# Optimization experiments

Hardware: AMD Instinct MI355X
Metric: run time of the kernel (lower is better)

## Reference

```python
import jax, jax.numpy as jnp
import numpy as np

VOCAB = 128
N_LAYERS = 4
HEAD_DIM = 128
N_HEADS = 16
PAD = 127
HIDDEN = N_HEADS * HEAD_DIM
B, S = 1, 2048
SCALE = 1.0 / float(np.sqrt(HEAD_DIM))


def _intervals(boundary):
    # torch: interval = cumsum(boundary)+1; shifted = roll(1); shifted[:,0]=interval[:,0]
    idx = jnp.cumsum(boundary.astype(jnp.int32), axis=-1) + 1
    sh = jnp.roll(idx, 1, axis=-1)
    return sh.at[:, 0].set(idx[:, 0])


def _build_mask(tokens, segment_mask, specials_mask):
    # Combined causal & padding & word & segment mask, cache_size=0, distances=0.
    word_int = _intervals(specials_mask)            # [B,S]
    seg_bound = ~segment_mask                       # [B,S]
    seg_int = _intervals(seg_bound)                 # [B,S]
    q = jnp.arange(S)[:, None]
    kv = jnp.arange(S)[None, :]
    causal = q >= kv                                # [S,S]
    dist_neg = (q - kv) < 0                         # mask_*_distance = 0 term
    nonpad = tokens != PAD                          # [B,S]
    padm = nonpad[:, :, None] & nonpad[:, None, :]  # [B,S,S]
    wordm = specials_mask[:, None, :] | dist_neg[None] | (word_int[:, :, None] == word_int[:, None, :])
    segm = seg_bound[:, None, :] | dist_neg[None] | (seg_int[:, :, None] == seg_int[:, None, :])
    return causal[None] & padm & wordm & segm       # [B,S,S]


def _attention(h, mask):
    # q=k=v=h (no projections in DummyModel); flex_attention default scale 1/sqrt(D)
    x = h.reshape(B, S, N_HEADS, HEAD_DIM)
    scores = jnp.einsum('bqhd,bkhd->bhqk', x, x) * SCALE
    neg = jnp.finfo(scores.dtype).min
    scores = jnp.where(mask[:, None], scores, neg)
    probs = jax.nn.softmax(scores, axis=-1)
    # fully-masked rows (e.g. padding queries) -> zero output, matching flex_attention
    row_valid = jnp.any(mask, axis=-1)              # [B,S]
    probs = jnp.where(row_valid[:, None, :, None], probs, 0.0)
    out = jnp.einsum('bhqk,bkhd->bqhd', probs, x)
    return out.reshape(B, S, HIDDEN)


def setup_inputs() -> dict:
    key = jax.random.key(0)
    k1, k2, k3, k4, k5, k6 = jax.random.split(key, 6)
    tokens = jax.random.randint(k1, (B, S), 0, PAD)          # 0..126, no pad tokens
    segment_mask = jax.random.bernoulli(k2, 0.98, (B, S))
    specials_mask = jax.random.bernoulli(k3, 0.2, (B, S))    # True = word boundary/special
    emb_w = jax.random.normal(k4, (VOCAB, HIDDEN), jnp.float32) * 0.02
    lm_w = jax.random.normal(k5, (VOCAB, HIDDEN), jnp.float32) * 0.02
    lm_b = jnp.zeros((VOCAB,), jnp.float32)
    seg_w = jax.random.normal(k6, (2, HIDDEN), jnp.float32) * 0.02
    seg_b = jnp.zeros((2,), jnp.float32)
    return {"tokens": tokens, "segment_mask": segment_mask, "specials_mask": specials_mask,
            "emb_w": emb_w, "lm_w": lm_w, "lm_b": lm_b, "seg_w": seg_w, "seg_b": seg_b}


def reference(tokens, segment_mask, specials_mask, emb_w, lm_w, lm_b, seg_w, seg_b):
    mask = _build_mask(tokens, segment_mask, specials_mask)
    hidden = emb_w[tokens]                                   # [B,S,HIDDEN]
    for _ in range(N_LAYERS):
        hidden = _attention(hidden, mask)
    logits = hidden @ lm_w.T + lm_b                          # [B,S,VOCAB]
    logits_segment = hidden @ seg_w.T + seg_b                # [B,S,2]
    return logits, logits_segment
```

## Files before the change

kernel.cpp:

```cpp
#include <hip/hip_runtime.h>

#define S 2048
#define HID 2048
#define NH 16
#define DH 128
#define VOC 128
#define LCAP 128
#define K2EXP 0.12752551286084112f
#define RTHR 62.0f
#define NEGS -3.0e38f

typedef __bf16 bf16_t;
typedef __attribute__((ext_vector_type(8))) __bf16 bf16x8;
typedef __attribute__((ext_vector_type(4))) __bf16 bf16x4;
typedef __attribute__((ext_vector_type(4))) float f32x4;
typedef __attribute__((ext_vector_type(16))) float f32x16;

typedef __attribute__((address_space(1))) unsigned int guint;
typedef __attribute__((address_space(3))) unsigned int luint;

#define MFMA16 __builtin_amdgcn_mfma_f32_16x16x32_bf16
#define MFMA32 __builtin_amdgcn_mfma_f32_32x32x16_bf16

__device__ __forceinline__ void gl_lds16(const void* g, void* l) {
  __builtin_amdgcn_global_load_lds((guint*)(unsigned long long)g,
                                   (luint*)(unsigned)(unsigned long long)l,
                                   16, 0, 0);
}

__device__ __forceinline__ unsigned cvtpk(float lo, float hi) {
  unsigned r;
  asm("v_cvt_pk_bf16_f32 %0, %1, %2" : "=v"(r) : "v"(lo), "v"(hi));
  return r;
}
__device__ __forceinline__ void plswap(unsigned& a, unsigned& b) {
  asm volatile("v_permlane32_swap_b32 %0, %1" : "+v"(a), "+v"(b));
}
__device__ __forceinline__ bf16x8 mk8(unsigned d0, unsigned d1, unsigned d2, unsigned d3) {
  union { unsigned u[4]; bf16x8 v; } x;
  x.u[0] = d0; x.u[1] = d1; x.u[2] = d2; x.u[3] = d3;
  return x.v;
}

__global__ __launch_bounds__(256) void maskprep2(const int* __restrict__ tokens,
                                                 const unsigned char* __restrict__ seg,
                                                 const unsigned char* __restrict__ spc,
                                                 int4* __restrict__ mi,
                                                 int* __restrict__ lq,
                                                 unsigned long long* __restrict__ lmask,
                                                 int2* __restrict__ smeta) {
  __shared__ int ssp[257], ssg[257], smw[257], sms[257], sfl[257];
  __shared__ int fpre[2048];
  __shared__ int ns64[64];
  __shared__ unsigned long long lmk[32];
  __shared__ int cdet[2];
  int t = threadIdx.x;
  if (t < 2) cdet[t] = 0;
  if (t < 32) lmk[t] = 0ull;
  __syncthreads();
  {
    int nz = ((t & 3) != 0 && seg[t]) ? 1 : 0;
    int fc = ((t & 3) == 3 && seg[t] == 0x3f) ? 1 : 0;
    if (nz) atomicAdd(&cdet[0], 1);
    if (fc) atomicAdd(&cdet[1], 1);
  }
  __syncthreads();
  int lay = (cdet[1] > 8) ? 2 : ((cdet[0] > 4) ? 1 : 0);
  auto getb = [&](const unsigned char* p, int i) -> int {
    if (lay == 1) return p[i] != 0;
    if (lay == 2) return ((const float*)p)[i] != 0.f;
    return ((const int*)p)[i] != 0;
  };
  int base = t * 8;
  int spv[8], sgv[8], npv[8], fv[8];
  int a = 0, b = 0, mw = 0, ms = 0, fs = 0;
  for (int j = 0; j < 8; j++) {
    int i = base + j;
    spv[j] = getb(spc, i);
    sgv[j] = 1 - getb(seg, i);
    npv[j] = (tokens[i] != 127) ? 1 : 0;
    fv[j] = spv[j] & sgv[j] & npv[j];
    a += spv[j]; b += sgv[j]; fs += fv[j];
    if (i >= 1 && spv[j]) mw = (i + 1 > mw) ? i + 1 : mw;
    if (i >= 1 && sgv[j]) ms = (i + 1 > ms) ? i + 1 : ms;
  }
  ssp[t + 1] = a; ssg[t + 1] = b; smw[t + 1] = mw; sms[t + 1] = ms; sfl[t + 1] = fs;
  if (t == 0) { ssp[0] = 0; ssg[0] = 0; smw[0] = 0; sms[0] = 0; sfl[0] = 0; }
  __syncthreads();
  for (int off = 1; off < 256; off <<= 1) {
    int v0 = 0, v1 = 0, v2 = 0, v3 = 0, v4 = 0;
    if (t + 1 > off) { v0 = ssp[t+1-off]; v1 = ssg[t+1-off]; v2 = smw[t+1-off]; v3 = sms[t+1-off]; v4 = sfl[t+1-off]; }
    __syncthreads();
    ssp[t + 1] += v0; ssg[t + 1] += v1;
    if (v2 > smw[t + 1]) smw[t + 1] = v2;
    if (v3 > sms[t + 1]) sms[t + 1] = v3;
    sfl[t + 1] += v4;
    __syncthreads();
  }
  if ((t & 3) == 0) {
    int ws = smw[t], ss = sms[t];
    ns64[t >> 2] = ws < ss ? ws : ss;
  }
  int esp = ssp[t], esg = ssg[t], ef = sfl[t];
  for (int j = 0; j < 8; j++) {
    int i = base + j;
    int wint = (i == 0) ? (1 + spv[j]) : (1 + esp);
    int sint = (i == 0) ? (1 + sgv[j]) : (1 + esg);
    mi[i] = make_int4(npv[j] | (spv[j] << 1) | (sgv[j] << 2), wint, sint, 0);
    fpre[i] = ef;
    int lqv = (fv[j] && ef < LCAP) ? ef : -1;
    lq[i] = lqv;
    if (lqv >= 0) atomicOr(&lmk[i >> 6], 1ull << (i & 63));
    esp += spv[j]; esg += sgv[j]; ef += fv[j];
  }
  __syncthreads();
  if (t < 32) lmask[t] = lmk[t];
  if (t < 64) {
    int nsTile = ns64[t] >> 5;
    int lc = fpre[nsTile * 32];
    if (lc > LCAP) lc = LCAP;
    smeta[t] = make_int2(nsTile, lc);
  }
}

__global__ __launch_bounds__(256) void bitgen(const int4* __restrict__ mi,
                                              unsigned* __restrict__ cmask) {
  __shared__ int4 km[32];
  int w = blockIdx.x;
  int t = threadIdx.x;
  int q = blockIdx.y * 256 + t;
  if (t < 32) km[t] = mi[w * 32 + t];
  __syncthreads();
  int4 mq = mi[q];
  unsigned word = 0;
  #pragma unroll
  for (int j = 0; j < 32; j++) {
    int kv = w * 32 + j;
    int4 mk = km[j];
    bool v = ((mq.x & mk.x) & 1) &&
             ((mk.x & 2) || (mq.y == mk.y)) &&
             ((mk.x & 4) || (mq.z == mk.z)) &&
             (kv <= q);
    word |= (v ? 1u : 0u) << j;
  }
  cmask[(size_t)w * S + q] = word;
}

__device__ __forceinline__ void store_h_hT(bf16x8 ob[4], bf16_t* tile, int q0, int h,
                                           int ql, int d0, int tid,
                                           bf16_t* __restrict__ hb, bf16_t* __restrict__ hbT) {
  #pragma unroll
  for (int i = 0; i < 4; i++)
    *(bf16x8*)(hb + (size_t)(q0 + ql) * HID + h * DH + d0 + i * 8) = ob[i];
  #pragma unroll
  for (int i = 0; i < 4; i++)
    #pragma unroll
    for (int j = 0; j < 8; j++) tile[ql * 136 + d0 + i * 8 + j] = ob[i][j];
  __syncthreads();
  int dT = tid >> 1, qh = (tid & 1) * 32;
  bf16x8 tb[4];
  #pragma unroll
  for (int i = 0; i < 4; i++)
    #pragma unroll
    for (int j = 0; j < 8; j++) tb[i][j] = tile[(qh + i * 8 + j) * 136 + dT];
  #pragma unroll
  for (int i = 0; i < 4; i++)
    *(bf16x8*)(hbT + (size_t)(h * DH + dT) * S + q0 + qh + i * 8) = tb[i];
}

__global__ __launch_bounds__(256) void embedT(const int* __restrict__ tokens,
                                              const float* __restrict__ emb,
                                              const int* __restrict__ lq,
                                              const unsigned long long* __restrict__ lmask,
                                              bf16_t* __restrict__ hb, bf16_t* __restrict__ hbT,
                                              bf16_t* __restrict__ hbL, bf16_t* __restrict__ hbLT) {
  __shared__ bf16_t tile[64 * 136];
  int tid = threadIdx.x;
  int q0 = blockIdx.x * 64, h = blockIdx.y;
  int ql = tid >> 2, d0 = (tid & 3) * 32;
  int tok = tokens[q0 + ql];
  const float4* src = (const float4*)(emb + (size_t)tok * HID + h * DH + d0);
  bf16x8 ob[4];
  #pragma unroll
  for (int i = 0; i < 8; i++) {
    float4 f = src[i];
    ob[i >> 1][(i & 1) * 4 + 0] = (bf16_t)f.x;
    ob[i >> 1][(i & 1) * 4 + 1] = (bf16_t)f.y;
    ob[i >> 1][(i & 1) * 4 + 2] = (bf16_t)f.z;
    ob[i >> 1][(i & 1) * 4 + 3] = (bf16_t)f.w;
  }
  store_h_hT(ob, tile, q0, h, ql, d0, tid, hb, hbT);
  unsigned long long lm = lmask[q0 >> 6];
  while (lm) {
    int r = __builtin_ctzll(lm);
    lm &= lm - 1;
    int li = lq[q0 + r];
    if (li >= 0 && tid < 128) {
      bf16_t vv = tile[r * 136 + tid];
      hbL[(size_t)li * HID + h * DH + tid] = vv;
      hbLT[((size_t)(h * DH + tid)) * LCAP + li] = vv;
    }
  }
}

__global__ __launch_bounds__(64, 2) void attn7(const bf16_t* __restrict__ hb,
                                               const bf16_t* __restrict__ hbT,
                                               const bf16_t* __restrict__ hbL,
                                               const bf16_t* __restrict__ hbLT,
                                               const unsigned* __restrict__ cmask,
                                               const int4* __restrict__ mi,
                                               const int2* __restrict__ smeta,
                                               const int* __restrict__ lq,
                                               const unsigned long long* __restrict__ lmask,
                                               bf16_t* __restrict__ ob,
                                               bf16_t* __restrict__ obT,
                                               bf16_t* __restrict__ obL,
                                               bf16_t* __restrict__ obLT,
                                               int writeT) {
  __shared__ __align__(16) char lds_raw[32768];

  int h = blockIdx.x, st = blockIdx.y;
  int2 sm = smeta[st];
  int nsT = sm.x, lcount = sm.y;
  int nNear = st + 1 - nsT;
  int nLT = (lcount + 31) >> 5;
  int nIter = nNear + nLT;

  int l = threadIdx.x, l31 = l & 31, hi = l >> 5;
  int q0 = 32 * st, q = q0 + l31;
  int npq = mi[q].x & 1;

  bf16x8 qf[8];
  {
    const bf16_t* hq = hb + (size_t)q * HID + h * DH;
    #pragma unroll
    for (int ks = 0; ks < 8; ks++) qf[ks] = *(const bf16x8*)(hq + ks * 16 + hi * 8);
  }

  f32x16 acc[4];
  #pragma unroll
  for (int i = 0; i < 4; i++)
    #pragma unroll
    for (int r = 0; r < 16; r++) acc[i][r] = 0.f;
  float m = -1e30f, lsum = 0.f;
  int swz = l31 & 7;

  auto STAGE = [&](int i, int b) {
    const bf16_t* Kbase; const bf16_t* Vbase; size_t Vstr;
    if (i < nNear) {
      int kv0 = (nsT + i) * 32;
      Kbase = hb + (size_t)kv0 * HID + h * DH;
      Vbase = hbT + (size_t)(h * DH) * S + kv0; Vstr = S;
    } else {
      int j0 = (i - nNear) * 32;
      Kbase = hbL + (size_t)j0 * HID + h * DH;
      Vbase = hbLT + (size_t)(h * DH) * LCAP + j0; Vstr = LCAP;
    }
    bf16_t* Kb = (bf16_t*)(lds_raw + b * 16384);
    bf16_t* Vb = (bf16_t*)(lds_raw + b * 16384 + 8192);
    #pragma unroll
    for (int i2 = 0; i2 < 8; i2++) {
      int rowK = i2 * 4 + (l >> 4); int chK = (l & 15) ^ (rowK & 7);
      gl_lds16(Kbase + (size_t)rowK * HID + chK * 8, Kb + i2 * 512);
    }
    #pragma unroll
    for (int i2 = 0; i2 < 8; i2++) {
      int rowV = i2 * 16 + (l >> 2); int chV = (l & 3) ^ (rowV & 3);
      gl_lds16(Vbase + (size_t)rowV * Vstr + chV * 8, Vb + i2 * 512);
    }
  };

  auto getmask = [&](int i) -> unsigned {
    if (i < nNear) return cmask[(size_t)(nsT + i) * S + q];
    int rem = lcount - (i - nNear) * 32;
    unsigned w0 = (rem >= 32) ? 0xffffffffu : ((rem <= 0) ? 0u : ((1u << rem) - 1u));
    return npq ? w0 : 0u;
  };

  STAGE(0, 0);
  for (int i = 0; i < nIter; i++) {
    int b = i & 1;
    if (i + 1 < nIter) {
      STAGE(i + 1, b ^ 1);
      asm volatile("s_waitcnt vmcnt(16)" ::: "memory");
    } else {
      asm volatile("s_waitcnt vmcnt(0)" ::: "memory");
    }
    unsigned w0 = getmask(i);

    if (__any(w0 != 0u)) {
      const bf16_t* Kb = (const bf16_t*)(lds_raw + b * 16384);
      const bf16_t* Vb = (const bf16_t*)(lds_raw + b * 16384 + 8192);
      f32x16 s;
      #pragma unroll
      for (int r = 0; r < 16; r++) s[r] = 0.f;
      const bf16_t* kp = Kb + l31 * 128;
      #pragma unroll
      for (int ks = 0; ks < 8; ks++) {
        bf16x8 kf = *(const bf16x8*)(kp + (((2 * ks + hi) ^ swz) * 8));
        s = MFMA32(kf, qf[ks], s, 0, 0, 0);
      }

      float sv[16];
      float mx = NEGS;
      #pragma unroll
      for (int r = 0; r < 16; r++) {
        int bit = (r & 3) + 8 * (r >> 2) + 4 * hi;
        sv[r] = ((w0 >> bit) & 1u) ? s[r] : NEGS;
        mx = fmaxf(mx, sv[r]);
      }
      mx = fmaxf(mx, __shfl_xor(mx, 32, 64));
      if (__any(mx > m + RTHR)) {
        float mn = fmaxf(m, mx);
        float al = exp2f((m - mn) * K2EXP);
        m = mn; lsum *= al;
        #pragma unroll
        for (int r = 0; r < 16; r++) {
          float alr = __shfl(al, (r & 3) + 8 * (r >> 2) + 4 * hi, 64);
          #pragma unroll
          for (int d = 0; d < 4; d++) acc[d][r] *= alr;
        }
      }
      float mk = m * K2EXP;
      float p[16], ps = 0.f;
      #pragma unroll
      for (int r = 0; r < 16; r++) {
        p[r] = exp2f(__builtin_fmaf(sv[r], K2EXP, -mk));
        ps += p[r];
      }
      ps += __shfl_xor(ps, 32, 64);
      lsum += ps;

      bf16x8 pa[2];
      {
        unsigned a0 = cvtpk(p[0], p[1]),   a1 = cvtpk(p[2], p[3]);
        unsigned b0 = cvtpk(p[4], p[5]),   b1 = cvtpk(p[6], p[7]);
        unsigned a2 = cvtpk(p[8], p[9]),   a3 = cvtpk(p[10], p[11]);
        unsigned b2 = cvtpk(p[12], p[13]), b3 = cvtpk(p[14], p[15]);
        plswap(a0, b0); plswap(a1, b1); plswap(a2, b2); plswap(a3, b3);
        pa[0] = mk8(a0, a1, b0, b1);
        pa[1] = mk8(a2, a3, b2, b3);
      }

      #pragma unroll
      for (int db = 0; db < 4; db++) {
        const bf16_t* vr = Vb + (32 * db + l31) * 32;
        #pragma unroll
        for (int ks = 0; ks < 2; ks++) {
          bf16x8 vf = *(const bf16x8*)(vr + (((2 * ks + hi) ^ (l31 & 3)) * 8));
          acc[db] = MFMA32(pa[ks], vf, acc[db], 0, 0, 0);
        }
      }
    }
  }

  bf16_t* tl = (bf16_t*)lds_raw;
  float inv = (lsum > 0.f) ? 1.f / lsum : 0.f;
  #pragma unroll
  for (int r = 0; r < 16; r++) {
    int qr = (r & 3) + 8 * (r >> 2) + 4 * hi;
    float ivr = __shfl(inv, qr, 64);
    #pragma unroll
    for (int db = 0; db < 4; db++)
      tl[qr * 132 + db * 32 + l31] = (bf16_t)(acc[db][r] * ivr);
  }
  {
    int row = l >> 1, hf = l & 1;
    #pragma unroll
    for (int k = 0; k < 8; k++) {
      bf16x8 v = *(const bf16x8*)(tl + row * 132 + hf * 64 + k * 8);
      *(bf16x8*)(ob + (size_t)(q0 + row) * HID + h * DH + hf * 64 + k * 8) = v;
    }
  }
  if (writeT) {
    #pragma unroll
    for (int half = 0; half < 2; half++) {
      int dd = l + 64 * half;
      #pragma unroll
      for (int c = 0; c < 4; c++) {
        bf16x8 v;
        #pragma unroll
        for (int e = 0; e < 8; e++) v[e] = tl[(c * 8 + e) * 132 + dd];
        *(bf16x8*)(obT + (size_t)(h * DH + dd) * S + q0 + c * 8) = v;
      }
    }
    unsigned lm32 = (unsigned)(lmask[st >> 1] >> ((st & 1) * 32));
    while (lm32) {
      int r = __builtin_ctz(lm32);
      lm32 &= lm32 - 1;
      int li = lq[q0 + r];
      if (li >= 0) {
        #pragma unroll
        for (int half = 0; half < 2; half++) {
          int dd = l + 64 * half;
          bf16_t vv = tl[r * 132 + dd];
          obL[(size_t)li * HID + h * DH + dd] = vv;
          obLT[((size_t)(h * DH + dd)) * LCAP + li] = vv;
        }
      }
    }
  }
}

__global__ __launch_bounds__(256) void wcvt(const float* __restrict__ w, bf16_t* __restrict__ wb) {
  int i = blockIdx.x * 256 + threadIdx.x;
  float4 f = ((const float4*)w)[i];
  bf16x4 v;
  v[0] = (bf16_t)f.x; v[1] = (bf16_t)f.y; v[2] = (bf16_t)f.z; v[3] = (bf16_t)f.w;
  *(bf16x4*)(wb + (size_t)i * 4) = v;
}

__global__ __launch_bounds__(256) void lmseg_head(const bf16_t* __restrict__ hb,
                                                  const bf16_t* __restrict__ wbf,
                                                  const float* __restrict__ bias,
                                                  const float* __restrict__ sw,
                                                  const float* __restrict__ sb,
                                                  float* __restrict__ out,
                                                  float* __restrict__ outseg) {
  __shared__ float red[4][16][130];
  int tid = threadIdx.x;
  int w = tid >> 6, l = tid & 63, l16 = l & 15, g = l >> 4;
  int t0 = blockIdx.x * 16;
  f32x4 acc[8];
  #pragma unroll
  for (int i = 0; i < 8; i++) acc[i] = (f32x4){0.f, 0.f, 0.f, 0.f};
  const bf16_t* arow = hb + (size_t)(t0 + l16) * HID + w * 512;
  for (int k0 = 0; k0 < 512; k0 += 32) {
    bf16x8 af = *(const bf16x8*)(arow + k0 + g * 8);
    #pragma unroll
    for (int vt = 0; vt < 8; vt++) {
      bf16x8 bf_ = *(const bf16x8*)(wbf + (size_t)(vt * 16 + l16) * HID + w * 512 + k0 + g * 8);
      acc[vt] = MFMA16(af, bf_, acc[vt], 0, 0, 0);
    }
  }
  #pragma unroll
  for (int vt = 0; vt < 8; vt++)
    #pragma unroll
    for (int r = 0; r < 4; r++)
      red[w][4 * g + r][vt * 16 + l16] = acc[vt][r];
  __syncthreads();
  int q = tid >> 4, vc = (tid & 15) * 8;
  #pragma unroll
  for (int j = 0; j < 8; j++) {
    float s = red[0][q][vc + j] + red[1][q][vc + j] + red[2][q][vc + j] + red[3][q][vc + j];
    out[(size_t)(t0 + q) * VOC + vc + j] = s + bias[vc + j];
  }
  {
    int c = tid & 15;
    const bf16_t* hrow = hb + (size_t)(t0 + q) * HID + c * 128;
    float s0 = 0.f, s1 = 0.f;
    #pragma unroll
    for (int i = 0; i < 16; i++) {
      bf16x8 v = *(const bf16x8*)(hrow + i * 8);
      const float4* w0p = (const float4*)(sw + c * 128 + i * 8);
      const float4* w1p = (const float4*)(sw + HID + c * 128 + i * 8);
      float4 x0 = w0p[0], x1 = w0p[1], y0 = w1p[0], y1 = w1p[1];
      s0 += (float)v[0]*x0.x + (float)v[1]*x0.y + (float)v[2]*x0.z + (float)v[3]*x0.w
          + (float)v[4]*x1.x + (float)v[5]*x1.y + (float)v[6]*x1.z + (float)v[7]*x1.w;
      s1 += (float)v[0]*y0.x + (float)v[1]*y0.y + (float)v[2]*y0.z + (float)v[3]*y0.w
          + (float)v[4]*y1.x + (float)v[5]*y1.y + (float)v[6]*y1.z + (float)v[7]*y1.w;
    }
    #pragma unroll
    for (int off = 1; off < 16; off <<= 1) {
      s0 += __shfl_xor(s0, off, 64);
      s1 += __shfl_xor(s1, off, 64);
    }
    if (c == 0) {
      outseg[(size_t)(t0 + q) * 2] = s0 + sb[0];
      outseg[(size_t)(t0 + q) * 2 + 1] = s1 + sb[1];
    }
  }
}

extern "C" void kernel_launch(void* const* d_in, const int* in_sizes, int n_in,
                              void* d_out, int out_size, void* d_ws, size_t ws_size,
                              hipStream_t stream) {
  const int* tokens = (const int*)d_in[0];
  const unsigned char* seg = (const unsigned char*)d_in[1];
  const unsigned char* spc = (const unsigned char*)d_in[2];
  const float* emb_w = (const float*)d_in[3];
  const float* lm_w = (const float*)d_in[4];
  const float* lm_b = (const float*)d_in[5];
  const float* seg_w = (const float*)d_in[6];
  const float* seg_b = (const float*)d_in[7];

  char* ws = (char*)d_ws;
  int4* mi = (int4*)ws;
  unsigned* cmask = (unsigned*)(ws + (1u << 20));
  int* lq = (int*)(ws + (1u << 20) + (512u << 10));
  unsigned long long* lmask = (unsigned long long*)(ws + (1u << 20) + (520u << 10));
  int2* smeta = (int2*)(ws + (1u << 20) + (524u << 10));
  bf16_t* wbf = (bf16_t*)(ws + (2u << 20));
  bf16_t* hbLA  = (bf16_t*)(ws + (3u << 20));
  bf16_t* hbLTA = (bf16_t*)(ws + (3u << 20) + (512u << 10));
  bf16_t* hbLB  = (bf16_t*)(ws + (4u << 20));
  bf16_t* hbLTB = (bf16_t*)(ws + (4u << 20) + (512u << 10));
  bf16_t* hbA  = (bf16_t*)(ws + (8u << 20));
  bf16_t* hbTA = (bf16_t*)(ws + (16u << 20));
  bf16_t* hbB  = (bf16_t*)(ws + (24u << 20));
  bf16_t* hbTB = (bf16_t*)(ws + (32u << 20));
  float* out = (float*)d_out;

  maskprep2<<<1, 256, 0, stream>>>(tokens, seg, spc, mi, lq, lmask, smeta);
  bitgen<<<dim3(64, 8), 256, 0, stream>>>(mi, cmask);
  embedT<<<dim3(S / 64, NH), 256, 0, stream>>>(tokens, emb_w, lq, lmask, hbA, hbTA, hbLA, hbLTA);

  bf16_t* cur = hbA;   bf16_t* curT = hbTA;
  bf16_t* nxt = hbB;   bf16_t* nxtT = hbTB;
  bf16_t* curL = hbLA; bf16_t* curLT = hbLTA;
  bf16_t* nxtL = hbLB; bf16_t* nxtLT = hbLTB;
  for (int L = 0; L < 4; L++) {
    attn7<<<dim3(NH, 64), 64, 0, stream>>>(cur, curT, curL, curLT, cmask, mi, smeta, lq, lmask,
                                           nxt, nxtT, nxtL, nxtLT, (L < 3) ? 1 : 0);
    bf16_t* t1 = cur; cur = nxt; nxt = t1;
    bf16_t* t2 = curT; curT = nxtT; nxtT = t2;
    bf16_t* t3 = curL; curL = nxtL; nxtL = t3;
    bf16_t* t4 = curLT; curLT = nxtLT; nxtLT = t4;
  }

  wcvt<<<(VOC * HID / 4) / 256, 256, 0, stream>>>(lm_w, wbf);
  lmseg_head<<<S / 16, 256, 0, stream>>>(cur, wbf, lm_b, seg_w, seg_b, out, out + (size_t)S * VOC);
}
```

Measured before the change: 147.6 us.

## Store V as pre-swizzled contiguous 32x128 tiles per head

Replaces the globally transposed hidden-state copy (hbT, stride S) with a tiled layout in which each head's 32-token V tile is stored contiguously, already in the XOR-swizzled LDS order. Attention staging then does linear 16-byte global-to-LDS loads instead of strided row gathers, and the producer kernels (embed and the attention epilogue) write tiles in that layout. The aim is better coalescing and fewer memory transactions for V loads. The cost is a more complex transpose-and-swizzle in the writers and a changed output store pattern.

```diff
diff --git a/kernel.cpp b/kernel.cpp
--- a/kernel.cpp
+++ b/kernel.cpp
@@ -41,6 +41,7 @@
   x.u[0] = d0; x.u[1] = d1; x.u[2] = d2; x.u[3] = d3;
   return x.v;
 }
+
 
 __global__ __launch_bounds__(256) void maskprep2(const int* __restrict__ tokens,
                                                  const unsigned char* __restrict__ seg,
@@ -146,34 +147,12 @@
   cmask[(size_t)w * S + q] = word;
 }
 
-__device__ __forceinline__ void store_h_hT(bf16x8 ob[4], bf16_t* tile, int q0, int h,
-                                           int ql, int d0, int tid,
-                                           bf16_t* __restrict__ hb, bf16_t* __restrict__ hbT) {
-  #pragma unroll
-  for (int i = 0; i < 4; i++)
-    *(bf16x8*)(hb + (size_t)(q0 + ql) * HID + h * DH + d0 + i * 8) = ob[i];
-  #pragma unroll
-  for (int i = 0; i < 4; i++)
-    #pragma unroll
-    for (int j = 0; j < 8; j++) tile[ql * 136 + d0 + i * 8 + j] = ob[i][j];
-  __syncthreads();
-  int dT = tid >> 1, qh = (tid & 1) * 32;
-  bf16x8 tb[4];
-  #pragma unroll
-  for (int i = 0; i < 4; i++)
-    #pragma unroll
-    for (int j = 0; j < 8; j++) tb[i][j] = tile[(qh + i * 8 + j) * 136 + dT];
-  #pragma unroll
-  for (int i = 0; i < 4; i++)
-    *(bf16x8*)(hbT + (size_t)(h * DH + dT) * S + q0 + qh + i * 8) = tb[i];
-}
-
-__global__ __launch_bounds__(256) void embedT(const int* __restrict__ tokens,
-                                              const float* __restrict__ emb,
-                                              const int* __restrict__ lq,
-                                              const unsigned long long* __restrict__ lmask,
-                                              bf16_t* __restrict__ hb, bf16_t* __restrict__ hbT,
-                                              bf16_t* __restrict__ hbL, bf16_t* __restrict__ hbLT) {
+__global__ __launch_bounds__(256) void embedT2(const int* __restrict__ tokens,
+                                               const float* __restrict__ emb,
+                                               const int* __restrict__ lq,
+                                               const unsigned long long* __restrict__ lmask,
+                                               bf16_t* __restrict__ hb, bf16_t* __restrict__ vtb,
+                                               bf16_t* __restrict__ hbL, bf16_t* __restrict__ vtbL) {
   __shared__ bf16_t tile[64 * 136];
   int tid = threadIdx.x;
   int q0 = blockIdx.x * 64, h = blockIdx.y;
@@ -189,7 +168,26 @@
     ob[i >> 1][(i & 1) * 4 + 2] = (bf16_t)f.z;
     ob[i >> 1][(i & 1) * 4 + 3] = (bf16_t)f.w;
   }
-  store_h_hT(ob, tile, q0, h, ql, d0, tid, hb, hbT);
+  #pragma unroll
+  for (int i = 0; i < 4; i++)
+    *(bf16x8*)(hb + (size_t)(q0 + ql) * HID + h * DH + d0 + i * 8) = ob[i];
+  #pragma unroll
+  for (int i = 0; i < 4; i++)
+    #pragma unroll
+    for (int j = 0; j < 8; j++) tile[ql * 136 + d0 + i * 8 + j] = ob[i][j];
+  __syncthreads();
+  {
+    int tl = tid >> 7, d = tid & 127;
+    bf16_t* vt = vtb + ((size_t)(h * 64) + 2 * blockIdx.x + tl) * 4096;
+    #pragma unroll
+    for (int c = 0; c < 4; c++) {
+      bf16x8 v;
+      #pragma unroll
+      for (int e = 0; e < 8; e++)
+        v[e] = tile[(32 * tl + 8 * (c ^ (d & 3)) + e) * 136 + d];
+      *(bf16x8*)(vt + d * 32 + c * 8) = v;
+    }
+  }
   unsigned long long lm = lmask[q0 >> 6];
   while (lm) {
     int r = __builtin_ctzll(lm);
@@ -198,24 +196,24 @@
     if (li >= 0 && tid < 128) {
       bf16_t vv = tile[r * 136 + tid];
       hbL[(size_t)li * HID + h * DH + tid] = vv;
-      hbLT[((size_t)(h * DH + tid)) * LCAP + li] = vv;
-    }
-  }
-}
-
-__global__ __launch_bounds__(64, 2) void attn7(const bf16_t* __restrict__ hb,
-                                               const bf16_t* __restrict__ hbT,
+      vtbL[((size_t)(h * 4) + (li >> 5)) * 4096 + tid * 32 + (((li & 31) >> 3) ^ (tid & 3)) * 8 + (li & 7)] = vv;
+    }
+  }
+}
+
+__global__ __launch_bounds__(64, 2) void attn8(const bf16_t* __restrict__ hb,
+                                               const bf16_t* __restrict__ vtb,
                                                const bf16_t* __restrict__ hbL,
-                                               const bf16_t* __restrict__ hbLT,
+                                               const bf16_t* __restrict__ vtbL,
                                                const unsigned* __restrict__ cmask,
                                                const int4* __restrict__ mi,
                                                const int2* __restrict__ smeta,
                                                const int* __restrict__ lq,
                                                const unsigned long long* __restrict__ lmask,
                                                bf16_t* __restrict__ ob,
-                                               bf16_t* __restrict__ obT,
+                                               bf16_t* __restrict__ ovtb,
                                                bf16_t* __restrict__ obL,
-                                               bf16_t* __restrict__ obLT,
+                                               bf16_t* __restrict__ ovtbL,
                                                int writeT) {
   __shared__ __align__(16) char lds_raw[32768];
 
@@ -246,15 +244,15 @@
   int swz = l31 & 7;
 
   auto STAGE = [&](int i, int b) {
-    const bf16_t* Kbase; const bf16_t* Vbase; size_t Vstr;
+    const bf16_t* Kbase; const bf16_t* Vtile;
     if (i < nNear) {
-      int kv0 = (nsT + i) * 32;
-      Kbase = hb + (size_t)kv0 * HID + h * DH;
-      Vbase = hbT + (size_t)(h * DH) * S + kv0; Vstr = S;
+      int t = nsT + i;
+      Kbase = hb + (size_t)(t * 32) * HID + h * DH;
+      Vtile = vtb + ((size_t)(h * 64) + t) * 4096;
     } else {
-      int j0 = (i - nNear) * 32;
-      Kbase = hbL + (size_t)j0 * HID + h * DH;
-      Vbase = hbLT + (size_t)(h * DH) * LCAP + j0; Vstr = LCAP;
+      int j = i - nNear;
+      Kbase = hbL + (size_t)(j * 32) * HID + h * DH;
+      Vtile = vtbL + ((size_t)(h * 4) + j) * 4096;
     }
     bf16_t* Kb = (bf16_t*)(lds_raw + b * 16384);
     bf16_t* Vb = (bf16_t*)(lds_raw + b * 16384 + 8192);
@@ -264,10 +262,8 @@
       gl_lds16(Kbase + (size_t)rowK * HID + chK * 8, Kb + i2 * 512);
     }
     #pragma unroll
-    for (int i2 = 0; i2 < 8; i2++) {
-      int rowV = i2 * 16 + (l >> 2); int chV = (l & 3) ^ (rowV & 3);
-      gl_lds16(Vbase + (size_t)rowV * Vstr + chV * 8, Vb + i2 * 512);
-    }
+    for (int i2 = 0; i2 < 8; i2++)
+      gl_lds16(Vtile + i2 * 512 + l * 8, Vb + i2 * 512);
   };
 
   auto getmask = [&](int i) -> unsigned {
@@ -365,24 +361,27 @@
       tl[qr * 132 + db * 32 + l31] = (bf16_t)(acc[db][r] * ivr);
   }
   {
-    int row = l >> 1, hf = l & 1;
-    #pragma unroll
-    for (int k = 0; k < 8; k++) {
-      bf16x8 v = *(const bf16x8*)(tl + row * 132 + hf * 64 + k * 8);
-      *(bf16x8*)(ob + (size_t)(q0 + row) * HID + h * DH + hf * 64 + k * 8) = v;
+    int c4 = l & 3;
+    #pragma unroll
+    for (int g = 0; g < 2; g++) {
+      int row = g * 16 + (l >> 2);
+      #pragma unroll
+      for (int k = 0; k < 4; k++) {
+        bf16x8 v = *(const bf16x8*)(tl + row * 132 + c4 * 32 + k * 8);
+        *(bf16x8*)(ob + (size_t)(q0 + row) * HID + h * DH + c4 * 32 + k * 8) = v;
+      }
     }
   }
   if (writeT) {
-    #pragma unroll
-    for (int half = 0; half < 2; half++) {
-      int dd = l + 64 * half;
-      #pragma unroll
-      for (int c = 0; c < 4; c++) {
-        bf16x8 v;
-        #pragma unroll
-        for (int e = 0; e < 8; e++) v[e] = tl[(c * 8 + e) * 132 + dd];
-        *(bf16x8*)(obT + (size_t)(h * DH + dd) * S + q0 + c * 8) = v;
-      }
+    bf16_t* vt = ovtb + ((size_t)(h * 64) + st) * 4096;
+    #pragma unroll
+    for (int s = 0; s < 8; s++) {
+      int d = s * 16 + (l >> 2);
+      bf16x8 v;
+      #pragma unroll
+      for (int e = 0; e < 8; e++)
+        v[e] = tl[(8 * ((l & 3) ^ (d & 3)) + e) * 132 + d];
+      *(bf16x8*)(vt + s * 512 + l * 8) = v;
     }
     unsigned lm32 = (unsigned)(lmask[st >> 1] >> ((st & 1) * 32));
     while (lm32) {
@@ -395,7 +394,7 @@
           int dd = l + 64 * half;
           bf16_t vv = tl[r * 132 + dd];
           obL[(size_t)li * HID + h * DH + dd] = vv;
-          obLT[((size_t)(h * DH + dd)) * LCAP + li] = vv;
+          ovtbL[((size_t)(h * 4) + (li >> 5)) * 4096 + dd * 32 + (((li & 31) >> 3) ^ (dd & 3)) * 8 + (li & 7)] = vv;
         }
       }
     }
@@ -492,30 +491,30 @@
   int2* smeta = (int2*)(ws + (1u << 20) + (524u << 10));
   bf16_t* wbf = (bf16_t*)(ws + (2u << 20));
   bf16_t* hbLA  = (bf16_t*)(ws + (3u << 20));
-  bf16_t* hbLTA = (bf16_t*)(ws + (3u << 20) + (512u << 10));
-  bf16_t* hbLB  = (bf16_t*)(ws + (4u << 20));
-  bf16_t* hbLTB = (bf16_t*)(ws + (4u << 20) + (512u << 10));
+  bf16_t* hbLB  = (bf16_t*)(ws + (3u << 20) + (512u << 10));
+  bf16_t* vtbLA = (bf16_t*)(ws + (4u << 20));
+  bf16_t* vtbLB = (bf16_t*)(ws + (4u << 20) + (512u << 10));
   bf16_t* hbA  = (bf16_t*)(ws + (8u << 20));
-  bf16_t* hbTA = (bf16_t*)(ws + (16u << 20));
-  bf16_t* hbB  = (bf16_t*)(ws + (24u << 20));
-  bf16_t* hbTB = (bf16_t*)(ws + (32u << 20));
+  bf16_t* hbB  = (bf16_t*)(ws + (16u << 20));
+  bf16_t* vtbA = (bf16_t*)(ws + (24u << 20));
+  bf16_t* vtbB = (bf16_t*)(ws + (32u << 20));
   float* out = (float*)d_out;
 
   maskprep2<<<1, 256, 0, stream>>>(tokens, seg, spc, mi, lq, lmask, smeta);
   bitgen<<<dim3(64, 8), 256, 0, stream>>>(mi, cmask);
-  embedT<<<dim3(S / 64, NH), 256, 0, stream>>>(tokens, emb_w, lq, lmask, hbA, hbTA, hbLA, hbLTA);
-
-  bf16_t* cur = hbA;   bf16_t* curT = hbTA;
-  bf16_t* nxt = hbB;   bf16_t* nxtT = hbTB;
-  bf16_t* curL = hbLA; bf16_t* curLT = hbLTA;
-  bf16_t* nxtL = hbLB; bf16_t* nxtLT = hbLTB;
+  embedT2<<<dim3(S / 64, NH), 256, 0, stream>>>(tokens, emb_w, lq, lmask, hbA, vtbA, hbLA, vtbLA);
+
+  bf16_t* cur = hbA;   bf16_t* curV = vtbA;
+  bf16_t* nxt = hbB;   bf16_t* nxtV = vtbB;
+  bf16_t* curL = hbLA; bf16_t* curLV = vtbLA;
+  bf16_t* nxtL = hbLB; bf16_t* nxtLV = vtbLB;
   for (int L = 0; L < 4; L++) {
-    attn7<<<dim3(NH, 64), 64, 0, stream>>>(cur, curT, curL, curLT, cmask, mi, smeta, lq, lmask,
-                                           nxt, nxtT, nxtL, nxtLT, (L < 3) ? 1 : 0);
+    attn8<<<dim3(NH, 64), 64, 0, stream>>>(cur, curV, curL, curLV, cmask, mi, smeta, lq, lmask,
+                                           nxt, nxtV, nxtL, nxtLV, (L < 3) ? 1 : 0);
     bf16_t* t1 = cur; cur = nxt; nxt = t1;
-    bf16_t* t2 = curT; curT = nxtT; nxtT = t2;
+    bf16_t* t2 = curV; curV = nxtV; nxtV = t2;
     bf16_t* t3 = curL; curL = nxtL; nxtL = t3;
-    bf16_t* t4 = curLT; curLT = nxtLT; nxtLT = t4;
+    bf16_t* t4 = curLV; curLV = nxtLV; nxtLV = t4;
   }
 
   wcvt<<<(VOC * HID / 4) / 256, 256, 0, stream>>>(lm_w, wbf);
```

New measurement: 137.3 us. -7.0%, faster.
